# Optimization experiments

Hardware: AMD Instinct MI355X
Metric: run time of the kernel (lower is better)

Reference implementation:

```python
import jax, jax.numpy as jnp
import numpy as np

B, T, C = 2, 2048, 1024
N_HEAD = 16
HEAD = C // N_HEAD


def setup_inputs() -> dict:
    key = jax.random.key(0)
    k1, k2, k3 = jax.random.split(key, 3)
    x = jax.random.normal(k1, (B, T, C), dtype=jnp.float32)
    w_qkv = jax.random.normal(k2, (3 * C, C), dtype=jnp.float32) * 0.02
    w_proj = jax.random.normal(k3, (C, C), dtype=jnp.float32) * 0.02
    return {"x": x, "w_qkv": w_qkv, "w_proj": w_proj}


def reference(x, w_qkv, w_proj):
    b, t, c = x.shape
    # c_attn: y = x @ W^T  (no bias). Split rows of W into q/k/v blocks.
    wq, wk, wv = jnp.split(w_qkv, 3, axis=0)            # each [C, C]
    q = (x @ wq.T).reshape(b, t, N_HEAD, HEAD)          # [B,T,H,D]
    k = (x @ wk.T).reshape(b, t, N_HEAD, HEAD)
    v = (x @ wv.T).reshape(b, t, N_HEAD, HEAD)
    scale = 1.0 / np.sqrt(HEAD).astype(np.float32)
    scores = jnp.einsum('bqhd,bkhd->bhqk', q, k) * scale  # [B,H,T,T]
    causal = jnp.tril(jnp.ones((t, t), dtype=bool))
    scores = jnp.where(causal, scores, -jnp.inf)
    attn = jax.nn.softmax(scores, axis=-1)               # [B,H,T,T]
    out = jnp.einsum('bhqk,bkhd->bqhd', attn, v).reshape(b, t, c)
    return out @ w_proj.T
```

## Files before the change

### kernel.cpp

```cpp
#include <hip/hip_runtime.h>
#include <hip/hip_bf16.h>


typedef __attribute__((ext_vector_type(8))) short bf16x8;
typedef __attribute__((ext_vector_type(4))) short bf16x4;
typedef __attribute__((ext_vector_type(4))) float floatx4;
typedef __attribute__((ext_vector_type(16))) float f32x16;

#define MFMA16(a, b, c) __builtin_amdgcn_mfma_f32_16x16x32_bf16((a), (b), (c), 0, 0, 0)
#define MFMA32(a, b, c) __builtin_amdgcn_mfma_f32_32x32x16_bf16((a), (b), (c), 0, 0, 0)

#if __has_builtin(__builtin_amdgcn_exp2f)
#define EXP2F(x) __builtin_amdgcn_exp2f(x)
#else
#define EXP2F(x) exp2f(x)
#endif

static constexpr int Bc = 2, Tc = 2048, Cc = 1024, Hc = 16, Dc = 64;
static constexpr size_t QKV_STRIDE = (size_t)Bc * Hc * Tc * Dc;
static constexpr float KSL2E = 0.125f * 1.44269504088896f;

__device__ __forceinline__ bf16x8 load8(const __hip_bfloat16* p) {
    return *(const bf16x8*)p;
}

__device__ __forceinline__ short f2b(float x) {
    union { __hip_bfloat16 h; short s; } u;
    u.h = __float2bfloat16(x);
    return u.s;
}

__device__ __forceinline__ bf16x8 pack8(floatx4 a, floatx4 b) {
    bf16x8 r;
    r[0] = f2b(a[0]); r[1] = f2b(a[1]); r[2] = f2b(a[2]); r[3] = f2b(a[3]);
    r[4] = f2b(b[0]); r[5] = f2b(b[1]); r[6] = f2b(b[2]); r[7] = f2b(b[3]);
    return r;
}

__device__ __forceinline__ unsigned pk2(float a, float b) {
    return (unsigned)(unsigned short)f2b(a) |
           ((unsigned)(unsigned short)f2b(b) << 16);
}

__device__ __forceinline__ void pl32swap(unsigned& a, unsigned& b) {
    asm volatile("v_permlane32_swap_b32 %0, %1" : "+v"(a), "+v"(b));
}

__device__ __forceinline__ bf16x8 mk8(unsigned a, unsigned b, unsigned c, unsigned d) {
    union { unsigned u[4]; bf16x8 v; } x;
    x.u[0] = a; x.u[1] = b; x.u[2] = c; x.u[3] = d;
    return x.v;
}

__device__ __forceinline__ void gl2lds16(const void* g, void* l) {
    __builtin_amdgcn_global_load_lds(
        (const __attribute__((address_space(1))) void*)g,
        (__attribute__((address_space(3))) void*)l, 16, 0, 0);
}

__global__ __launch_bounds__(256) void cvt_bf16(
    const float* __restrict__ in, __hip_bfloat16* __restrict__ out, int n8) {
    const int i = blockIdx.x * 256 + threadIdx.x;
    if (i < n8) {
        const floatx4 a = *(const floatx4*)&in[(size_t)i * 8];
        const floatx4 b = *(const floatx4*)&in[(size_t)i * 8 + 4];
        *(bf16x8*)&out[(size_t)i * 8] = pack8(a, b);
    }
}

__global__ __launch_bounds__(256) void gemm_qkv_bf16(
    const __hip_bfloat16* __restrict__ A,
    const __hip_bfloat16* __restrict__ W,
    __hip_bfloat16* __restrict__ qkv) {
    __shared__ __hip_bfloat16 As16[128 * 32];
    __shared__ __hip_bfloat16 Bs16[128 * 32];
    const int K = Cc;
    const int lane = threadIdx.x & 63;
    const int wave = threadIdx.x >> 6;
    const int waveM = wave >> 1, waveN = wave & 1;
    const int flat = blockIdx.y * 32 + blockIdx.x;
    const int swz = (flat & 7) * 96 + (flat >> 3);
    const int mBase = (swz & 31) * 128;
    const int nBase = (swz >> 5) * 128;
    const int idx16 = lane & 15;
    const int quad = lane >> 4;
    const int aRow = lane >> 2, aPos = lane & 3;

    floatx4 acc[4][4] = {};

    for (int k0 = 0; k0 < K; k0 += 32) {
        __syncthreads();
#pragma unroll
        for (int s = 0; s < 2; s++) {
            const int r0 = wave * 32 + s * 16;
            const int row = r0 + aRow;
            const int cg = aPos ^ (row & 3);
            gl2lds16(A + (size_t)(mBase + row) * K + k0 + cg * 8, &As16[r0 * 32]);
            gl2lds16(W + (size_t)(nBase + row) * K + k0 + cg * 8, &Bs16[r0 * 32]);
        }
        __syncthreads();

        bf16x8 af[4], bfr[4];
#pragma unroll
        for (int i = 0; i < 4; i++) {
            const int rr = waveM * 64 + i * 16 + idx16;
            af[i] = *(const bf16x8*)&As16[rr * 32 + ((quad ^ (rr & 3)) * 8)];
        }
#pragma unroll
        for (int j = 0; j < 4; j++) {
            const int rr = waveN * 64 + j * 16 + idx16;
            bfr[j] = *(const bf16x8*)&Bs16[rr * 32 + ((quad ^ (rr & 3)) * 8)];
        }
#pragma unroll
        for (int i = 0; i < 4; i++)
#pragma unroll
            for (int j = 0; j < 4; j++)
                acc[i][j] = MFMA16(af[i], bfr[j], acc[i][j]);
    }

#pragma unroll
    for (int i = 0; i < 4; i++) {
#pragma unroll
        for (int j = 0; j < 4; j++) {
            const int n = nBase + waveN * 64 + j * 16 + idx16;
            const int part = n >> 10;
            const int rem = n & 1023;
            const int h = rem >> 6, d = rem & 63;
#pragma unroll
            for (int r = 0; r < 4; r++) {
                const int m = mBase + waveM * 64 + i * 16 + quad * 4 + r;
                const int bb = m >> 11, t = m & 2047;
                const size_t o = (size_t)part * QKV_STRIDE +
                                 (((size_t)(bb * Hc + h)) * Tc + t) * Dc + d;
                qkv[o] = __float2bfloat16(acc[i][j][r]);
            }
        }
    }
}

__global__ __launch_bounds__(256) void gemm_proj_bf16(
    const __hip_bfloat16* __restrict__ A,
    const __hip_bfloat16* __restrict__ W,
    float* __restrict__ out) {
    __shared__ __hip_bfloat16 As16[128 * 32];
    __shared__ __hip_bfloat16 Bs16[64 * 32];
    const int K = Cc;
    const int lane = threadIdx.x & 63;
    const int wave = threadIdx.x >> 6;
    const int waveM = wave >> 1, waveN = wave & 1;
    const int mBase = blockIdx.x * 128;
    const int nBase = blockIdx.y * 64;
    const int idx16 = lane & 15;
    const int quad = lane >> 4;
    const int aRow = lane >> 2, aPos = lane & 3;

    floatx4 acc[4][2] = {};

    for (int k0 = 0; k0 < K; k0 += 32) {
        __syncthreads();
#pragma unroll
        for (int s = 0; s < 2; s++) {
            const int r0 = wave * 32 + s * 16;
            const int row = r0 + aRow;
            const int cg = aPos ^ (row & 3);
            gl2lds16(A + (size_t)(mBase + row) * K + k0 + cg * 8, &As16[r0 * 32]);
        }
        {
            const int r0 = wave * 16;
            const int row = r0 + aRow;
            const int cg = aPos ^ (row & 3);
            gl2lds16(W + (size_t)(nBase + row) * K + k0 + cg * 8, &Bs16[r0 * 32]);
        }
        __syncthreads();

        bf16x8 af[4], bfr[2];
#pragma unroll
        for (int i = 0; i < 4; i++) {
            const int rr = waveM * 64 + i * 16 + idx16;
            af[i] = *(const bf16x8*)&As16[rr * 32 + ((quad ^ (rr & 3)) * 8)];
        }
#pragma unroll
        for (int j = 0; j < 2; j++) {
            const int rr = waveN * 32 + j * 16 + idx16;
            bfr[j] = *(const bf16x8*)&Bs16[rr * 32 + ((quad ^ (rr & 3)) * 8)];
        }
#pragma unroll
        for (int i = 0; i < 4; i++)
#pragma unroll
            for (int j = 0; j < 2; j++)
                acc[i][j] = MFMA16(af[i], bfr[j], acc[i][j]);
    }

#pragma unroll
    for (int i = 0; i < 4; i++) {
#pragma unroll
        for (int j = 0; j < 2; j++) {
            const int n = nBase + waveN * 32 + j * 16 + idx16;
#pragma unroll
            for (int r = 0; r < 4; r++) {
                const int m = mBase + waveM * 64 + i * 16 + quad * 4 + r;
                out[(size_t)m * Cc + n] = acc[i][j][r];
            }
        }
    }
}

__global__ __launch_bounds__(256) void transpose_v(
    const __hip_bfloat16* __restrict__ v,
    __hip_bfloat16* __restrict__ vt) {
    __shared__ unsigned short tile[64][65];
    const int t0 = blockIdx.x * 64;
    const int h = blockIdx.y, b = blockIdx.z;
    const size_t base = ((size_t)(b * Hc + h)) * Tc * Dc;
    const unsigned short* vp = (const unsigned short*)v + base;
    unsigned short* vtp = (unsigned short*)vt + base;

    for (int e = threadIdx.x; e < 4096; e += 256) {
        const int tl = e >> 6, d = e & 63;
        tile[tl][d] = vp[(size_t)(t0 + tl) * Dc + d];
    }
    __syncthreads();
    for (int e = threadIdx.x; e < 4096; e += 256) {
        const int d = e >> 6, tl = e & 63;
        vtp[(size_t)d * Tc + t0 + tl] = tile[tl][d];
    }
}

__global__ __launch_bounds__(512) void attn_fold(
    const __hip_bfloat16* __restrict__ qkv,
    const __hip_bfloat16* __restrict__ vt,
    __hip_bfloat16* __restrict__ aout) {
    __shared__ floatx4 smem4[4096];
    char* const smem = (char*)smem4;
    __hip_bfloat16* const kA = (__hip_bfloat16*)smem;
    __hip_bfloat16* const vA = kA + 8192;
    __hip_bfloat16* const kB = vA + 8192;
    __hip_bfloat16* const vB = kB + 8192;
    float* const comb = (float*)smem;

    const int lane = threadIdx.x & 63;
    const int wave = threadIdx.x >> 6;
    const int c31 = lane & 31;
    const int hw = lane >> 5;
    const int p = blockIdx.x;
    const int h = blockIdx.y;
    const int b = blockIdx.z;
    const int H = 15 - p, L = p;
    const int lightEnd = 2 * p + 2;
    const int w3 = wave & 3;

    const size_t headOff = ((size_t)(b * Hc + h)) * Tc * Dc;
    const __hip_bfloat16* qp = qkv + headOff;
    const __hip_bfloat16* kp = qkv + QKV_STRIDE + headOff;
    const __hip_bfloat16* vtp = vt + headOff;

    int qB = ((wave < 4) ? H : L) * 128 + w3 * 32;
    int qtw = (qB + 31) >> 6;
    int qMax = qB + 31;
    int qg = qB + c31;

    bf16x8 qf0, qf1, qf2, qf3;
    auto loadQ = [&]() {
        const __hip_bfloat16* qr = qp + (size_t)qg * Dc + hw * 8;
        qf0 = load8(qr);
        qf1 = load8(qr + 16);
        qf2 = load8(qr + 32);
        qf3 = load8(qr + 48);
    };
    loadQ();

    f32x16 O0 = {}, O1 = {};
    float lacc = 0.f;

    auto stageA = [&](int kt, int buf) {
        const int keyBase = kt * 64;
#pragma unroll
        for (int s = 0; s < 2; s++) {
            const int blk = w3 * 2 + s;
            const int row = blk * 8 + (lane >> 3);
            const int g = (lane & 7) ^ (row & 7);
            gl2lds16(kp + (size_t)(keyBase + row) * Dc + g * 8,
                     kA + buf * 4096 + blk * 512);
            gl2lds16(vtp + (size_t)row * Tc + keyBase + g * 8,
                     vA + buf * 4096 + blk * 512);
        }
    };
    auto stageB = [&](int kt, int buf) {
        const int keyBase = kt * 64;
#pragma unroll
        for (int s = 0; s < 2; s++) {
            const int blk = w3 * 2 + s;
            const int row = blk * 8 + (lane >> 3);
            const int g = (lane & 7) ^ (row & 7);
            gl2lds16(kp + (size_t)(keyBase + row) * Dc + g * 8,
                     kB + buf * 4096 + blk * 512);
            gl2lds16(vtp + (size_t)row * Tc + keyBase + g * 8,
                     vB + buf * 4096 + blk * 512);
        }
    };

    auto computeTile = [&](const __hip_bfloat16* kS, const __hip_bfloat16* vS,
                           int keyBase, bool msk) {
#pragma unroll
        for (int kb = 0; kb < 2; kb++) {
            if (keyBase + kb * 32 <= qMax) {
                const int kr = kb * 32 + c31;
                const int m8 = kr & 7;
                f32x16 S = {};
                S = MFMA32(load8(&kS[kr * 64 + (((0 + hw) ^ m8) * 8)]), qf0, S);
                S = MFMA32(load8(&kS[kr * 64 + (((2 + hw) ^ m8) * 8)]), qf1, S);
                S = MFMA32(load8(&kS[kr * 64 + (((4 + hw) ^ m8) * 8)]), qf2, S);
                S = MFMA32(load8(&kS[kr * 64 + (((6 + hw) ^ m8) * 8)]), qf3, S);

                unsigned w[8];
                if (msk) {
#pragma unroll
                    for (int r = 0; r < 16; r += 2) {
                        const int key0 = keyBase + kb * 32 +
                                         (r & 3) + 8 * (r >> 2) + 4 * hw;
                        float p0 = EXP2F(S[r] * KSL2E);
                        p0 = (key0 > qg) ? 0.f : p0;
                        float p1 = EXP2F(S[r + 1] * KSL2E);
                        p1 = (key0 + 1 > qg) ? 0.f : p1;
                        lacc += p0 + p1;
                        w[r >> 1] = pk2(p0, p1);
                    }
                } else {
#pragma unroll
                    for (int r = 0; r < 16; r += 2) {
                        const float p0 = EXP2F(S[r] * KSL2E);
                        const float p1 = EXP2F(S[r + 1] * KSL2E);
                        lacc += p0 + p1;
                        w[r >> 1] = pk2(p0, p1);
                    }
                }
                pl32swap(w[0], w[2]);
                pl32swap(w[1], w[3]);
                pl32swap(w[4], w[6]);
                pl32swap(w[5], w[7]);
                const bf16x8 pA0 = mk8(w[0], w[1], w[2], w[3]);
                const bf16x8 pA1 = mk8(w[4], w[5], w[6], w[7]);

                {
                    const int vr = c31;
                    const int vm = vr & 7;
                    const bf16x8 vf0 = load8(&vS[vr * 64 + (((kb * 4 + hw) ^ vm) * 8)]);
                    const bf16x8 vf1 = load8(&vS[vr * 64 + (((kb * 4 + 2 + hw) ^ vm) * 8)]);
                    O0 = MFMA32(pA0, vf0, O0);
                    O0 = MFMA32(pA1, vf1, O0);
                }
                {
                    const int vr = 32 + c31;
                    const int vm = vr & 7;
                    const bf16x8 vf0 = load8(&vS[vr * 64 + (((kb * 4 + hw) ^ vm) * 8)]);
                    const bf16x8 vf1 = load8(&vS[vr * 64 + (((kb * 4 + 2 + hw) ^ vm) * 8)]);
                    O1 = MFMA32(pA0, vf0, O1);
                    O1 = MFMA32(pA1, vf1, O1);
                }
            }
        }
    };

    auto outStore = [&](int qB_, float ltot) {
#pragma unroll
        for (int r = 0; r < 16; r++) {
            const int qrl = (r & 3) + 8 * (r >> 2) + 4 * hw;
            const float lr = __shfl(ltot, qrl, 64);
            const float inv = 1.0f / lr;
            const size_t rowOff = ((size_t)(b * Tc + qB_ + qrl)) * Cc + h * 64;
            aout[rowOff + c31] = __float2bfloat16(O0[r] * inv);
            aout[rowOff + 32 + c31] = __float2bfloat16(O1[r] * inv);
        }
    };

    if (wave < 4) stageA(0, 0);

    for (int i = 0; i < 17; i++) {
        __syncthreads();
        if (i < 16) {
            if (wave < 4) stageA(i + 1, (i + 1) & 1);
            else if (i + 1 >= lightEnd) stageB(i + 16 - 2 * p, (i + 1) & 1);
        }
        if (wave >= 4 && i == lightEnd) {
            outStore(qB, lacc + __shfl_xor(lacc, 32, 64));
#pragma unroll
            for (int r = 0; r < 16; r++) { O0[r] = 0.f; O1[r] = 0.f; }
            lacc = 0.f;
            qB = H * 128 + w3 * 32;
            qtw = (qB + 31) >> 6;
            qMax = qB + 31;
            qg = qB + c31;
            loadQ();
        }
        if (wave < 4) {
            computeTile(kA + (i & 1) * 4096, vA + (i & 1) * 4096, i * 64,
                        i * 64 + 63 > qB);
        } else if (i < lightEnd) {
            if (i <= qtw)
                computeTile(kA + (i & 1) * 4096, vA + (i & 1) * 4096, i * 64,
                            i * 64 + 63 > qB);
        } else {
            const int kt = i + 15 - 2 * p;
            if (kt <= qtw)
                computeTile(kB + (i & 1) * 4096, vB + (i & 1) * 4096, kt * 64,
                            kt * 64 + 63 > qB);
        }
    }
    __syncthreads();

    const float ltotOwn = lacc + __shfl_xor(lacc, 32, 64);
    if (wave >= 4) {
        float* c = comb + (size_t)(wave - 4) * 2112;
#pragma unroll
        for (int r = 0; r < 16; r++) {
            c[r * 64 + lane] = O0[r];
            c[(16 + r) * 64 + lane] = O1[r];
        }
        c[2048 + lane] = ltotOwn;
    }
    __syncthreads();
    if (wave < 4) {
        float* c = comb + (size_t)wave * 2112;
#pragma unroll
        for (int r = 0; r < 16; r++) {
            O0[r] += c[r * 64 + lane];
            O1[r] += c[(16 + r) * 64 + lane];
        }
        outStore(qB, ltotOwn + c[2048 + lane]);
    }
}

__global__ __launch_bounds__(256) void gemm_qkv(
    const float* __restrict__ A,
    const float* __restrict__ W,
    __hip_bfloat16* __restrict__ qkv) {
    __shared__ float As[128 * 32];
    __shared__ float Bs[128 * 32];
    const int K = Cc;
    const int lane = threadIdx.x & 63;
    const int wave = threadIdx.x >> 6;
    const int waveM = wave >> 1, waveN = wave & 1;
    const int mBase = blockIdx.x * 128;
    const int nBase = blockIdx.y * 128;
    const int idx16 = lane & 15;
    const int quad = lane >> 4;
    const int ldRow = lane >> 3;
    const int ldPos = lane & 7;

    floatx4 acc[4][4] = {};

    for (int k0 = 0; k0 < K; k0 += 32) {
        __syncthreads();
#pragma unroll
        for (int s = 0; s < 4; s++) {
            const int r0 = wave * 32 + s * 8;
            const int row = r0 + ldRow;
            const int cg = ldPos ^ (row & 7);
            gl2lds16(A + (size_t)(mBase + row) * K + k0 + cg * 4, &As[r0 * 32]);
            gl2lds16(W + (size_t)(nBase + row) * K + k0 + cg * 4, &Bs[r0 * 32]);
        }
        __syncthreads();

        bf16x8 af[4], bfr[4];
#pragma unroll
        for (int i = 0; i < 4; i++) {
            const int rr = waveM * 64 + i * 16 + idx16;
            const floatx4 a0 = *(const floatx4*)&As[rr * 32 + (((quad * 2) ^ (rr & 7)) * 4)];
            const floatx4 a1 = *(const floatx4*)&As[rr * 32 + (((quad * 2 + 1) ^ (rr & 7)) * 4)];
            af[i] = pack8(a0, a1);
        }
#pragma unroll
        for (int j = 0; j < 4; j++) {
            const int rr = waveN * 64 + j * 16 + idx16;
            const floatx4 b0 = *(const floatx4*)&Bs[rr * 32 + (((quad * 2) ^ (rr & 7)) * 4)];
            const floatx4 b1 = *(const floatx4*)&Bs[rr * 32 + (((quad * 2 + 1) ^ (rr & 7)) * 4)];
            bfr[j] = pack8(b0, b1);
        }
#pragma unroll
        for (int i = 0; i < 4; i++)
#pragma unroll
            for (int j = 0; j < 4; j++)
                acc[i][j] = MFMA16(af[i], bfr[j], acc[i][j]);
    }

#pragma unroll
    for (int i = 0; i < 4; i++) {
#pragma unroll
        for (int j = 0; j < 4; j++) {
            const int n = nBase + waveN * 64 + j * 16 + idx16;
            const int part = n >> 10;
            const int rem = n & 1023;
            const int h = rem >> 6, d = rem & 63;
#pragma unroll
            for (int r = 0; r < 4; r++) {
                const int m = mBase + waveM * 64 + i * 16 + quad * 4 + r;
                const int bb = m >> 11, t = m & 2047;
                const size_t o = (size_t)part * QKV_STRIDE +
                                 (((size_t)(bb * Hc + h)) * Tc + t) * Dc + d;
                qkv[o] = __float2bfloat16(acc[i][j][r]);
            }
        }
    }
}

__global__ __launch_bounds__(256) void gemm_proj(
    const __hip_bfloat16* __restrict__ A,
    const float* __restrict__ W,
    float* __restrict__ out) {
    __shared__ __hip_bfloat16 As16[128 * 32];
    __shared__ float Ws[64 * 32];
    const int K = Cc;
    const int lane = threadIdx.x & 63;
    const int wave = threadIdx.x >> 6;
    const int waveM = wave >> 1, waveN = wave & 1;
    const int mBase = blockIdx.x * 128;
    const int nBase = blockIdx.y * 64;
    const int idx16 = lane & 15;
    const int quad = lane >> 4;
    const int aRow = lane >> 2, aPos = lane & 3;
    const int wRow = lane >> 3, wPos = lane & 7;

    floatx4 acc[4][2] = {};

    for (int k0 = 0; k0 < K; k0 += 32) {
        __syncthreads();
#pragma unroll
        for (int s = 0; s < 2; s++) {
            {
                const int r0 = wave * 32 + s * 16;
                const int row = r0 + aRow;
                const int cg = aPos ^ (row & 3);
                gl2lds16(A + (size_t)(mBase + row) * K + k0 + cg * 8, &As16[r0 * 32]);
            }
            {
                const int r0 = wave * 16 + s * 8;
                const int row = r0 + wRow;
                const int cg = wPos ^ (row & 7);
                gl2lds16(W + (size_t)(nBase + row) * K + k0 + cg * 4, &Ws[r0 * 32]);
            }
        }
        __syncthreads();

        bf16x8 af[4], bfr[2];
#pragma unroll
        for (int i = 0; i < 4; i++) {
            const int rr = waveM * 64 + i * 16 + idx16;
            af[i] = *(const bf16x8*)&As16[rr * 32 + ((quad ^ (rr & 3)) * 8)];
        }
#pragma unroll
        for (int j = 0; j < 2; j++) {
            const int rr = waveN * 32 + j * 16 + idx16;
            const floatx4 b0 = *(const floatx4*)&Ws[rr * 32 + (((quad * 2) ^ (rr & 7)) * 4)];
            const floatx4 b1 = *(const floatx4*)&Ws[rr * 32 + (((quad * 2 + 1) ^ (rr & 7)) * 4)];
            bfr[j] = pack8(b0, b1);
        }
#pragma unroll
        for (int i = 0; i < 4; i++)
#pragma unroll
            for (int j = 0; j < 2; j++)
                acc[i][j] = MFMA16(af[i], bfr[j], acc[i][j]);
    }

#pragma unroll
    for (int i = 0; i < 4; i++) {
#pragma unroll
        for (int j = 0; j < 2; j++) {
            const int n = nBase + waveN * 32 + j * 16 + idx16;
#pragma unroll
            for (int r = 0; r < 4; r++) {
                const int m = mBase + waveM * 64 + i * 16 + quad * 4 + r;
                out[(size_t)m * Cc + n] = acc[i][j][r];
            }
        }
    }
}

extern "C" void kernel_launch(void* const* d_in, const int* in_sizes, int n_in,
                              void* d_out, int out_size, void* d_ws, size_t ws_size,
                              hipStream_t stream) {
    const float* x = nullptr;
    const float* w_qkv = nullptr;
    const float* w_proj = nullptr;
    for (int i = 0; i < n_in; i++) {
        if (in_sizes[i] == 4194304) x = (const float*)d_in[i];
        else if (in_sizes[i] == 3145728) w_qkv = (const float*)d_in[i];
        else if (in_sizes[i] == 1048576) w_proj = (const float*)d_in[i];
    }
    float* out = (float*)d_out;

    __hip_bfloat16* qkv = (__hip_bfloat16*)d_ws;
    __hip_bfloat16* vbuf = qkv + 2 * QKV_STRIDE;
    __hip_bfloat16* vt = qkv + 3 * QKV_STRIDE;
    __hip_bfloat16* ao = vbuf;

    const size_t CVT_OFF = 8 * QKV_STRIDE;
    const size_t NEED = CVT_OFF + (4194304 + 3145728) * sizeof(__hip_bfloat16);

    if (ws_size >= NEED) {
        __hip_bfloat16* xb = (__hip_bfloat16*)((char*)d_ws + CVT_OFF);
        __hip_bfloat16* wbq = xb + 4194304;
        __hip_bfloat16* wbp = qkv;

        cvt_bf16<<<dim3(4194304 / 8 / 256), 256, 0, stream>>>(x, xb, 4194304 / 8);
        cvt_bf16<<<dim3(3145728 / 8 / 256), 256, 0, stream>>>(w_qkv, wbq, 3145728 / 8);
        gemm_qkv_bf16<<<dim3(4096 / 128, 3072 / 128), 256, 0, stream>>>(xb, wbq, qkv);
        transpose_v<<<dim3(Tc / 64, Hc, Bc), 256, 0, stream>>>(vbuf, vt);
        attn_fold<<<dim3(8, Hc, Bc), 512, 0, stream>>>(qkv, vt, ao);
        cvt_bf16<<<dim3(1048576 / 8 / 256), 256, 0, stream>>>(w_proj, wbp, 1048576 / 8);
        gemm_proj_bf16<<<dim3(4096 / 128, 1024 / 64), 256, 0, stream>>>(ao, wbp, out);
    } else {
        gemm_qkv<<<dim3(4096 / 128, 3072 / 128), 256, 0, stream>>>(x, w_qkv, qkv);
        transpose_v<<<dim3(Tc / 64, Hc, Bc), 256, 0, stream>>>(vbuf, vt);
        attn_fold<<<dim3(8, Hc, Bc), 512, 0, stream>>>(qkv, vt, ao);
        gemm_proj<<<dim3(4096 / 128, 1024 / 64), 256, 0, stream>>>(ao, w_proj, out);
    }
}
```

Baseline: 181.1 us.

## Double-buffer LDS staging in QKV and projection GEMMs with XCD-aware tile mapping

Both bf16 GEMM kernels now keep two LDS buffers and issue the async global-to-LDS copy for the next K-slice right after the barrier. This lets the copy overlap with the MFMA work on the current slice and removes one barrier per iteration. Block-to-tile mapping is also rearranged so each XCD works on a contiguous group of M and N tiles, which is meant to improve L2 reuse; the projection GEMM gains this swizzle for the first time. The cost is doubled LDS use per block, which may lower occupancy, and correctness relies on the barrier also waiting for the outstanding async loads.

```diff
diff --git a/kernel.cpp b/kernel.cpp
--- a/kernel.cpp
+++ b/kernel.cpp
@@ -72,44 +72,52 @@
     const __hip_bfloat16* __restrict__ A,
     const __hip_bfloat16* __restrict__ W,
     __hip_bfloat16* __restrict__ qkv) {
-    __shared__ __hip_bfloat16 As16[128 * 32];
-    __shared__ __hip_bfloat16 Bs16[128 * 32];
+    __shared__ __hip_bfloat16 As16[2][128 * 32];
+    __shared__ __hip_bfloat16 Bs16[2][128 * 32];
     const int K = Cc;
     const int lane = threadIdx.x & 63;
     const int wave = threadIdx.x >> 6;
     const int waveM = wave >> 1, waveN = wave & 1;
     const int flat = blockIdx.y * 32 + blockIdx.x;
-    const int swz = (flat & 7) * 96 + (flat >> 3);
-    const int mBase = (swz & 31) * 128;
-    const int nBase = (swz >> 5) * 128;
+    const int xcd = flat & 7;
+    const int l = flat >> 3;
+    const int mTile = (xcd & 3) * 8 + (l & 7);
+    const int nTile = (xcd >> 2) * 12 + (l >> 3);
+    const int mBase = mTile * 128;
+    const int nBase = nTile * 128;
     const int idx16 = lane & 15;
     const int quad = lane >> 4;
     const int aRow = lane >> 2, aPos = lane & 3;
 
     floatx4 acc[4][4] = {};
 
-    for (int k0 = 0; k0 < K; k0 += 32) {
-        __syncthreads();
+    auto stage = [&](int k0, int buf) {
 #pragma unroll
         for (int s = 0; s < 2; s++) {
             const int r0 = wave * 32 + s * 16;
             const int row = r0 + aRow;
             const int cg = aPos ^ (row & 3);
-            gl2lds16(A + (size_t)(mBase + row) * K + k0 + cg * 8, &As16[r0 * 32]);
-            gl2lds16(W + (size_t)(nBase + row) * K + k0 + cg * 8, &Bs16[r0 * 32]);
-        }
+            gl2lds16(A + (size_t)(mBase + row) * K + k0 + cg * 8, &As16[buf][r0 * 32]);
+            gl2lds16(W + (size_t)(nBase + row) * K + k0 + cg * 8, &Bs16[buf][r0 * 32]);
+        }
+    };
+
+    stage(0, 0);
+    for (int k0 = 0; k0 < K; k0 += 32) {
+        const int buf = (k0 >> 5) & 1;
         __syncthreads();
+        if (k0 + 32 < K) stage(k0 + 32, buf ^ 1);
 
         bf16x8 af[4], bfr[4];
 #pragma unroll
         for (int i = 0; i < 4; i++) {
             const int rr = waveM * 64 + i * 16 + idx16;
-            af[i] = *(const bf16x8*)&As16[rr * 32 + ((quad ^ (rr & 3)) * 8)];
+            af[i] = *(const bf16x8*)&As16[buf][rr * 32 + ((quad ^ (rr & 3)) * 8)];
         }
 #pragma unroll
         for (int j = 0; j < 4; j++) {
             const int rr = waveN * 64 + j * 16 + idx16;
-            bfr[j] = *(const bf16x8*)&Bs16[rr * 32 + ((quad ^ (rr & 3)) * 8)];
+            bfr[j] = *(const bf16x8*)&Bs16[buf][rr * 32 + ((quad ^ (rr & 3)) * 8)];
         }
 #pragma unroll
         for (int i = 0; i < 4; i++)
@@ -142,47 +150,57 @@
     const __hip_bfloat16* __restrict__ A,
     const __hip_bfloat16* __restrict__ W,
     float* __restrict__ out) {
-    __shared__ __hip_bfloat16 As16[128 * 32];
-    __shared__ __hip_bfloat16 Bs16[64 * 32];
+    __shared__ __hip_bfloat16 As16[2][128 * 32];
+    __shared__ __hip_bfloat16 Bs16[2][64 * 32];
     const int K = Cc;
     const int lane = threadIdx.x & 63;
     const int wave = threadIdx.x >> 6;
     const int waveM = wave >> 1, waveN = wave & 1;
-    const int mBase = blockIdx.x * 128;
-    const int nBase = blockIdx.y * 64;
+    const int flat = blockIdx.y * 32 + blockIdx.x;
+    const int xcd = flat & 7;
+    const int l = flat >> 3;
+    const int mTile = (xcd & 3) * 8 + (l & 7);
+    const int nTile = (xcd >> 2) * 8 + (l >> 3);
+    const int mBase = mTile * 128;
+    const int nBase = nTile * 64;
     const int idx16 = lane & 15;
     const int quad = lane >> 4;
     const int aRow = lane >> 2, aPos = lane & 3;
 
     floatx4 acc[4][2] = {};
 
-    for (int k0 = 0; k0 < K; k0 += 32) {
-        __syncthreads();
+    auto stage = [&](int k0, int buf) {
 #pragma unroll
         for (int s = 0; s < 2; s++) {
             const int r0 = wave * 32 + s * 16;
             const int row = r0 + aRow;
             const int cg = aPos ^ (row & 3);
-            gl2lds16(A + (size_t)(mBase + row) * K + k0 + cg * 8, &As16[r0 * 32]);
+            gl2lds16(A + (size_t)(mBase + row) * K + k0 + cg * 8, &As16[buf][r0 * 32]);
         }
         {
             const int r0 = wave * 16;
             const int row = r0 + aRow;
             const int cg = aPos ^ (row & 3);
-            gl2lds16(W + (size_t)(nBase + row) * K + k0 + cg * 8, &Bs16[r0 * 32]);
-        }
+            gl2lds16(W + (size_t)(nBase + row) * K + k0 + cg * 8, &Bs16[buf][r0 * 32]);
+        }
+    };
+
+    stage(0, 0);
+    for (int k0 = 0; k0 < K; k0 += 32) {
+        const int buf = (k0 >> 5) & 1;
         __syncthreads();
+        if (k0 + 32 < K) stage(k0 + 32, buf ^ 1);
 
         bf16x8 af[4], bfr[2];
 #pragma unroll
         for (int i = 0; i < 4; i++) {
             const int rr = waveM * 64 + i * 16 + idx16;
-            af[i] = *(const bf16x8*)&As16[rr * 32 + ((quad ^ (rr & 3)) * 8)];
+            af[i] = *(const bf16x8*)&As16[buf][rr * 32 + ((quad ^ (rr & 3)) * 8)];
         }
 #pragma unroll
         for (int j = 0; j < 2; j++) {
             const int rr = waveN * 32 + j * 16 + idx16;
-            bfr[j] = *(const bf16x8*)&Bs16[rr * 32 + ((quad ^ (rr & 3)) * 8)];
+            bfr[j] = *(const bf16x8*)&Bs16[buf][rr * 32 + ((quad ^ (rr & 3)) * 8)];
         }
 #pragma unroll
         for (int i = 0; i < 4; i++)
```

Measured after the change: 183.9 us. No clear change (+1.5%).
